# Kernel optimization log

Measured on AMD Instinct MI355X. Metric: run time of the kernel, lower is better.

The kernel has to match this reference:

```python
import jax, jax.numpy as jnp
import numpy as np

IN_CH = 256
NUM_ANCHORS = 9
NUM_CLASSES = 80
FEAT_SHAPES = [(4, IN_CH, 100, 100), (4, IN_CH, 50, 50), (4, IN_CH, 25, 25), (4, IN_CH, 13, 13), (4, IN_CH, 7, 7)]


def conv3x3(x, w, b):
    # x: [N,C,H,W], w: [O,I,3,3] (OIHW), stride 1, SAME padding
    y = jax.lax.conv_general_dilated(x, w, window_strides=(1, 1), padding='SAME',
                                     dimension_numbers=('NCHW', 'OIHW', 'NCHW'))
    return y + b[None, :, None, None]


def head_branch(x, conv_w, conv_b, out_w, out_b, K):
    for i in range(4):
        x = jax.nn.relu(conv3x3(x, conv_w[i], conv_b[i]))
    y = conv3x3(x, out_w, out_b)
    N, AK, H, W = y.shape
    A = AK // K
    return y.reshape(N, A, K, H, W).transpose(0, 3, 4, 1, 2).reshape(N, H * W * A, K)


def setup_inputs() -> dict:
    key = jax.random.key(0)
    ks = jax.random.split(key, 16)
    inp = {}
    for i, shp in enumerate(FEAT_SHAPES):
        inp[f'feat{i}'] = jax.random.normal(ks[i], shp, dtype=jnp.float32)
    std = 0.01  # torch init: normal(std=0.01), zero bias
    inp['cls_conv_w'] = jax.random.normal(ks[5], (4, IN_CH, IN_CH, 3, 3), dtype=jnp.float32) * std
    inp['cls_conv_b'] = jnp.zeros((4, IN_CH), dtype=jnp.float32)
    inp['cls_out_w'] = jax.random.normal(ks[6], (NUM_ANCHORS * NUM_CLASSES, IN_CH, 3, 3), dtype=jnp.float32) * std
    prior = 0.01
    inp['cls_out_b'] = jnp.full((NUM_ANCHORS * NUM_CLASSES,), -np.log((1.0 - prior) / prior), dtype=jnp.float32)
    inp['reg_conv_w'] = jax.random.normal(ks[7], (4, IN_CH, IN_CH, 3, 3), dtype=jnp.float32) * std
    inp['reg_conv_b'] = jnp.zeros((4, IN_CH), dtype=jnp.float32)
    inp['reg_out_w'] = jax.random.normal(ks[8], (NUM_ANCHORS * 4, IN_CH, 3, 3), dtype=jnp.float32) * std
    inp['reg_out_b'] = jnp.zeros((NUM_ANCHORS * 4,), dtype=jnp.float32)
    return inp


def reference(feat0, feat1, feat2, feat3, feat4,
              cls_conv_w, cls_conv_b, cls_out_w, cls_out_b,
              reg_conv_w, reg_conv_b, reg_out_w, reg_out_b):
    feats = [feat0, feat1, feat2, feat3, feat4]
    cls_logits = jnp.concatenate(
        [head_branch(f, cls_conv_w, cls_conv_b, cls_out_w, cls_out_b, NUM_CLASSES) for f in feats], axis=1)
    bbox_regression = jnp.concatenate(
        [head_branch(f, reg_conv_w, reg_conv_b, reg_out_w, reg_out_b, 4) for f in feats], axis=1)
    return cls_logits, bbox_regression
```

## Files before the change

kernel.cpp:

```cpp
#include <hip/hip_runtime.h>


typedef __bf16 v8bf __attribute__((ext_vector_type(8)));
typedef float f32x4 __attribute__((ext_vector_type(4)));

__device__ __forceinline__ v8bf zero8() {
  v8bf v;
#pragma unroll
  for (int j = 0; j < 8; ++j) v[j] = (__bf16)0.0f;
  return v;
}

__device__ __forceinline__ void glds16(const void* g, void* l) {
  __builtin_amdgcn_global_load_lds((const __attribute__((address_space(1))) unsigned int*)g,
                                   (__attribute__((address_space(3))) unsigned int*)l, 16, 0, 0);
}

struct Geo { int W, H, HW, pbase, obC, obR, t; };
__device__ __forceinline__ Geo decode(int r) {
  Geo g;
  if (r < 105)      { g.W=100;g.H=100;g.HW=10000;g.pbase=0;     g.obC=0;       g.obR=0;      g.t=r; }
  else if (r < 132) { g.W=50; g.H=50; g.HW=2500; g.pbase=40000; g.obC=7200000; g.obR=360000; g.t=r-105; }
  else if (r < 139) { g.W=25; g.H=25; g.HW=625;  g.pbase=50000; g.obC=9000000; g.obR=450000; g.t=r-132; }
  else if (r < 141) { g.W=13; g.H=13; g.HW=169;  g.pbase=52500; g.obC=9450000; g.obR=472500; g.t=r-139; }
  else              { g.W=7;  g.H=7;  g.HW=49;   g.pbase=53176; g.obC=9571680; g.obR=478584; g.t=r-141; }
  return g;
}

__global__ __launch_bounds__(256)
void prep_in(const float* __restrict__ f0, const float* __restrict__ f1,
             const float* __restrict__ f2, const float* __restrict__ f3,
             const float* __restrict__ f4, __bf16* __restrict__ dst)
{
  int oct = blockIdx.x * 256 + threadIdx.x;
  if (oct >= 1707904) return;
  int el = oct << 3;
  int c0 = el & 255;
  int pix = el >> 8;
  const float* s; int HW, hw, n;
  if (pix < 40000)      { s = f0; HW = 10000; int p = pix;         n = p / 10000; hw = p - n * 10000; }
  else if (pix < 50000) { s = f1; HW = 2500;  int p = pix - 40000; n = p / 2500;  hw = p - n * 2500;  }
  else if (pix < 52500) { s = f2; HW = 625;   int p = pix - 50000; n = p / 625;   hw = p - n * 625;   }
  else if (pix < 53176) { s = f3; HW = 169;   int p = pix - 52500; n = p / 169;   hw = p - n * 169;   }
  else                  { s = f4; HW = 49;    int p = pix - 53176; n = p / 49;    hw = p - n * 49;    }
  const float* sp = s + (n * 256 + c0) * HW + hw;
  v8bf v;
#pragma unroll
  for (int j = 0; j < 8; ++j) v[j] = (__bf16)sp[j * HW];
  *(v8bf*)(dst + el) = v;
}

__global__ __launch_bounds__(256)
void prep_w_all(const float* __restrict__ cls_w, const float* __restrict__ reg_w,
                const float* __restrict__ cls_ow, const float* __restrict__ reg_ow,
                __bf16* __restrict__ wb)
{
  int t = blockIdx.x * 256 + threadIdx.x;
  const float* src; __bf16* dst; int CO, within;
  if (t < 589824) {
    int tensor = t / 73728; within = t % 73728;
    src = tensor < 4 ? cls_w + tensor * 589824 : reg_w + (tensor - 4) * 589824;
    dst = wb + (size_t)tensor * 589824; CO = 256;
  } else if (t < 811008) {
    within = t - 589824; src = cls_ow; dst = wb + 8 * 589824; CO = 720;
  } else {
    within = t - 811008; src = reg_ow; dst = wb + 8 * 589824 + 1769472; CO = 36;
  }
  int p = within & 3; int xx = within >> 2;
  int co = xx & 127; xx >>= 7;
  int tap = xx % 9; xx /= 9;
  int cc = xx & 7; int nt = xx >> 3;
  int l = p ^ ((co >> 1) & 3);
  int cog = nt * 128 + co;
  v8bf v = zero8();
  if (cog < CO) {
    const float* sp = src + ((size_t)cog * 256 + cc * 32 + l * 8) * 9 + tap;
#pragma unroll
    for (int j = 0; j < 8; ++j) v[j] = (__bf16)sp[j * 9];
  }
  *(v8bf*)(dst + ((size_t)(((nt * 8 + cc) * 9 + tap) * 128 + co) * 32 + p * 8)) = v;
}

__device__ __forceinline__ void conv_core(const char* __restrict__ wsbase,
    unsigned so, unsigned zpoff, const char* __restrict__ wnt,
    int W, int H, int p0, int npx, f32x4 (&acc)[3][4])
{
  __shared__ __align__(16) char ldsA[28672];
  __shared__ __align__(16) char ldsB[24576];
  const int Wp = W + 2;
  const int pend = p0 + npx - 1;
  const int rowlo = p0 / W - 1;
  const int tid = threadIdx.x, lane = tid & 63, wv = tid >> 6;
  const int wn = wv & 1, wm = wv >> 1, la = lane & 15, kg = lane >> 4;

  unsigned offA[7];
#pragma unroll
  for (int j = 0; j < 7; ++j) {
    int pos = (wv * 7 + j) * 16 + (lane >> 2);
    int h = pos / Wp;
    int wc = pos - h * Wp - 1;
    int ar = rowlo + h;
    int pl = (lane & 3) ^ ((pos >> 1) & 3);
    bool ok = (ar >= 0) & (ar < H) & (wc >= 0) & (wc < W);
    offA[j] = ok ? (so + (unsigned)(ar * W + wc) * 512u + (unsigned)pl * 16u)
                 : (zpoff + (unsigned)(lane & 3) * 16u);
  }

  int pos0[3], fvalid[3];
#pragma unroll
  for (int f = 0; f < 3; ++f) {
    int fg = wm * 3 + f;
    fvalid[f] = (fg * 16 < npx);
    int p = p0 + fg * 16 + la; if (p > pend) p = pend;
    int h = p / W;
    pos0[f] = (h - rowlo) * Wp + (p - h * W + 1);
  }

  int boff[4];
#pragma unroll
  for (int nj = 0; nj < 4; ++nj) {
    int co = wn * 64 + nj * 16 + la;
    boff[nj] = (co << 6) + ((kg << 4) ^ (((co >> 1) & 3) << 4));
  }

  const char* bq = wnt + wv * 2048 + lane * 16;
  char* bd = (char*)ldsB + wv * 2048;

#pragma unroll
  for (int j = 0; j < 7; ++j) { glds16(wsbase + offA[j], (char*)ldsA + (wv * 7 + j) * 1024); offA[j] += 64u; }
  glds16(bq, bd); glds16(bq + 1024, bd + 1024);
  glds16(bq + 8192, bd + 8192); glds16(bq + 9216, bd + 9216);

  for (int cc = 0; cc < 8; ++cc) {
#pragma unroll
    for (int tap = 0; tap < 9; ++tap) {
      if (tap == 8) {
        if (cc == 7) { asm volatile("s_waitcnt vmcnt(0)" ::: "memory"); }
        else         { asm volatile("s_waitcnt vmcnt(2)" ::: "memory"); }
      } else         { asm volatile("s_waitcnt vmcnt(2)" ::: "memory"); }
      __builtin_amdgcn_s_barrier();
      if (tap == 0 && cc > 0) {
#pragma unroll
        for (int j = 0; j < 7; ++j) { glds16(wsbase + offA[j], (char*)ldsA + (wv * 7 + j) * 1024); offA[j] += 64u; }
        const char* bs = bq + (cc * 9 + 2) * 8192;
        glds16(bs, bd + 16384); glds16(bs + 1024, bd + 17408);
        asm volatile("s_waitcnt vmcnt(2)" ::: "memory");
        __builtin_amdgcn_s_barrier();
      } else {
        int q = cc * 9 + tap;
        if (q < 70) {
          const char* bs = bq + (q + 2) * 8192;
          char* d = bd + ((tap + 2) % 3) * 8192;
          glds16(bs, d); glds16(bs + 1024, d + 1024);
        }
      }
      const char* bbuf = (const char*)ldsB + (tap % 3) * 8192;
      v8bf bfr[4];
#pragma unroll
      for (int nj = 0; nj < 4; ++nj) bfr[nj] = *(const v8bf*)(bbuf + boff[nj]);
      const int dh = tap / 3 - 1, dw = tap % 3 - 1;
      const int dt = dh * Wp + dw;
      v8bf afr[3];
#pragma unroll
      for (int f = 0; f < 3; ++f)
        if (fvalid[f]) {
          int pos = pos0[f] + dt;
          afr[f] = *(const v8bf*)((const char*)ldsA + ((pos << 6) + ((kg << 4) ^ (((pos >> 1) & 3) << 4))));
        }
      __builtin_amdgcn_s_setprio(1);
#pragma unroll
      for (int f = 0; f < 3; ++f)
        if (fvalid[f])
#pragma unroll
          for (int nj = 0; nj < 4; ++nj)
            acc[f][nj] = __builtin_amdgcn_mfma_f32_16x16x32_bf16(afr[f], bfr[nj], acc[f][nj], 0, 0, 0);
      __builtin_amdgcn_s_setprio(0);
    }
  }
}

__global__ __launch_bounds__(256, 3)
void conv_tower(const char* __restrict__ wsbase,
                unsigned so0, __bf16* __restrict__ dst0, const __bf16* __restrict__ w0, const float* __restrict__ b0,
                unsigned so1, __bf16* __restrict__ dst1, const __bf16* __restrict__ w1, const float* __restrict__ b1,
                unsigned zpoff, int nb)
{
  int bid = blockIdx.x;
  int br = (nb == 2 && bid >= 1136) ? 1 : 0;
  bid -= br * 1136;
  unsigned soff = br ? so1 : so0;
  __bf16* dst = br ? dst1 : dst0;
  const __bf16* wt = br ? w1 : w0;
  const float* bias = br ? b1 : b0;

  int x = bid & 7, slot = bid >> 3;
  int nt = slot & 1, mtl = slot >> 1;
  int mt = x + (mtl << 3);
  int n = mt / 142, r = mt - n * 142;
  Geo g = decode(r);
  int p0 = g.t * 96;
  int npx = g.HW - p0; if (npx > 96) npx = 96;
  unsigned so = soff + (unsigned)(g.pbase + n * g.HW) * 512u;

  f32x4 acc[3][4];
#pragma unroll
  for (int f = 0; f < 3; ++f)
#pragma unroll
    for (int j = 0; j < 4; ++j)
#pragma unroll
      for (int k = 0; k < 4; ++k) acc[f][j][k] = 0.0f;

  conv_core(wsbase, so, zpoff, (const char*)(wt + nt * 294912), g.W, g.H, p0, npx, acc);

  int lane = threadIdx.x & 63, wv = threadIdx.x >> 6;
  int wm = wv >> 1, wn = wv & 1, la = lane & 15, kg = lane >> 4;
  size_t pixbase = (size_t)(g.pbase + n * g.HW + p0);
#pragma unroll
  for (int f = 0; f < 3; ++f) {
    int fg = wm * 3 + f;
    if (fg * 16 < npx) {
#pragma unroll
      for (int nj = 0; nj < 4; ++nj) {
        int cob = nt * 128 + wn * 64 + nj * 16 + la;
        float bs = bias[cob];
#pragma unroll
        for (int rr = 0; rr < 4; ++rr) {
          int pl = fg * 16 + kg * 4 + rr;
          if (pl < npx)
            dst[((pixbase + pl) << 8) + cob] = (__bf16)fmaxf(acc[f][nj][rr] + bs, 0.0f);
        }
      }
    }
  }
}

__global__ __launch_bounds__(256, 3)
void conv_out(const char* __restrict__ wsbase, unsigned soC, unsigned soR,
              float* __restrict__ out, const __bf16* __restrict__ wco, const float* __restrict__ bco,
              const __bf16* __restrict__ wro, const float* __restrict__ bro,
              unsigned zpoff, int mode)
{
  int bid = blockIdx.x;
  int isreg;
  if (mode == 2) { isreg = bid >= 3408; bid -= isreg ? 3408 : 0; }
  else isreg = (mode == 0);

  int x = bid & 7, slot = bid >> 3;
  int nt, mtl;
  if (!isreg) { nt = slot % 6; mtl = slot / 6; } else { nt = 0; mtl = slot; }
  int mt = x + mtl * 8;
  int n = mt / 142, r = mt - n * 142;
  Geo g = decode(r);
  int p0 = g.t * 96;
  int npx = g.HW - p0; if (npx > 96) npx = 96;
  unsigned so = (isreg ? soR : soC) + (unsigned)(g.pbase + n * g.HW) * 512u;
  const __bf16* wnt = isreg ? wro : (wco + nt * 294912);

  f32x4 acc[3][4];
#pragma unroll
  for (int f = 0; f < 3; ++f)
#pragma unroll
    for (int j = 0; j < 4; ++j)
#pragma unroll
      for (int k = 0; k < 4; ++k) acc[f][j][k] = 0.0f;

  conv_core(wsbase, so, zpoff, (const char*)wnt, g.W, g.H, p0, npx, acc);

  int lane = threadIdx.x & 63, wv = threadIdx.x >> 6;
  int wm = wv >> 1, wn = wv & 1, la = lane & 15, kg = lane >> 4;
#pragma unroll
  for (int f = 0; f < 3; ++f) {
    int fg = wm * 3 + f;
    if (fg * 16 < npx) {
#pragma unroll
      for (int nj = 0; nj < 4; ++nj) {
        int cob = nt * 128 + wn * 64 + nj * 16 + la;
#pragma unroll
        for (int rr = 0; rr < 4; ++rr) {
          int pl = fg * 16 + kg * 4 + rr;
          if (pl < npx) {
            int pix = p0 + pl;
            if (!isreg) {
              if (cob < 720)
                out[(size_t)n * 9606960 + g.obC + (size_t)pix * 720 + cob] = acc[f][nj][rr] + bco[cob];
            } else {
              if (cob < 36)
                out[38427840 + (size_t)n * 480348 + g.obR + (size_t)pix * 36 + cob] = acc[f][nj][rr] + bro[cob];
            }
          }
        }
      }
    }
  }
}

extern "C" void kernel_launch(void* const* d_in, const int* in_sizes, int n_in,
                              void* d_out, int out_size, void* d_ws, size_t ws_size,
                              hipStream_t stream) {
  (void)in_sizes; (void)n_in; (void)out_size;
  const float* feat0 = (const float*)d_in[0];
  const float* feat1 = (const float*)d_in[1];
  const float* feat2 = (const float*)d_in[2];
  const float* feat3 = (const float*)d_in[3];
  const float* feat4 = (const float*)d_in[4];
  const float* cls_w  = (const float*)d_in[5];
  const float* cls_b  = (const float*)d_in[6];
  const float* cls_ow = (const float*)d_in[7];
  const float* cls_ob = (const float*)d_in[8];
  const float* reg_w  = (const float*)d_in[9];
  const float* reg_b  = (const float*)d_in[10];
  const float* reg_ow = (const float*)d_in[11];
  const float* reg_ob = (const float*)d_in[12];
  float* out = (float*)d_out;

  const size_t ACT = 13663232;
  const size_t WSEG = 6782976;
  const char* wsbase = (const char*)d_ws;
  __bf16* base = (__bf16*)d_ws;

  bool fused = ws_size >= (5 * ACT + WSEG + 4096) * 2;
  int nact = fused ? 5 : 3;
  __bf16* A = base + ACT;
  __bf16* B = base + 2 * ACT;
  __bf16* C = fused ? base + 3 * ACT : A;
  __bf16* D = fused ? base + 4 * ACT : B;
  __bf16* wb = base + nact * ACT;

  __bf16* w_cls[4], *w_reg[4];
  for (int li = 0; li < 4; ++li) { w_cls[li] = wb + (size_t)li * 589824; w_reg[li] = wb + (size_t)(4 + li) * 589824; }
  __bf16* wco = wb + 8 * 589824;
  __bf16* wro = wco + 1769472;
  __bf16* zp = wro + 294912;

  unsigned off_in = 0;
  unsigned off_A = (unsigned)(ACT * 2);
  unsigned off_B = (unsigned)(ACT * 4);
  unsigned off_C = fused ? (unsigned)(ACT * 6) : off_A;
  unsigned off_D = fused ? (unsigned)(ACT * 8) : off_B;
  unsigned off_zp = (unsigned)((nact * ACT + WSEG) * 2);

  hipMemsetAsync(zp, 0, 8192, stream);
  prep_in<<<6672, 256, 0, stream>>>(feat0, feat1, feat2, feat3, feat4, base);
  prep_w_all<<<3312, 256, 0, stream>>>(cls_w, reg_w, cls_ow, reg_ow, wb);

  if (fused) {
    conv_tower<<<2272, 256, 0, stream>>>(wsbase, off_in, A, w_cls[0], cls_b + 0,   off_in, C, w_reg[0], reg_b + 0,   off_zp, 2);
    conv_tower<<<2272, 256, 0, stream>>>(wsbase, off_A,  B, w_cls[1], cls_b + 256, off_C,  D, w_reg[1], reg_b + 256, off_zp, 2);
    conv_tower<<<2272, 256, 0, stream>>>(wsbase, off_B,  A, w_cls[2], cls_b + 512, off_D,  C, w_reg[2], reg_b + 512, off_zp, 2);
    conv_tower<<<2272, 256, 0, stream>>>(wsbase, off_A,  B, w_cls[3], cls_b + 768, off_C,  D, w_reg[3], reg_b + 768, off_zp, 2);
    conv_out<<<3976, 256, 0, stream>>>(wsbase, off_B, off_D, out, wco, cls_ob, wro, reg_ob, off_zp, 2);
  } else {
    conv_tower<<<1136, 256, 0, stream>>>(wsbase, off_in, A, w_cls[0], cls_b + 0,   0, A, w_cls[0], cls_b, off_zp, 1);
    conv_tower<<<1136, 256, 0, stream>>>(wsbase, off_A,  B, w_cls[1], cls_b + 256, 0, A, w_cls[0], cls_b, off_zp, 1);
    conv_tower<<<1136, 256, 0, stream>>>(wsbase, off_B,  A, w_cls[2], cls_b + 512, 0, A, w_cls[0], cls_b, off_zp, 1);
    conv_tower<<<1136, 256, 0, stream>>>(wsbase, off_A,  B, w_cls[3], cls_b + 768, 0, A, w_cls[0], cls_b, off_zp, 1);
    conv_out<<<3408, 256, 0, stream>>>(wsbase, off_B, off_B, out, wco, cls_ob, wro, reg_ob, off_zp, 1);
    conv_tower<<<1136, 256, 0, stream>>>(wsbase, off_in, A, w_reg[0], reg_b + 0,   0, A, w_reg[0], reg_b, off_zp, 1);
    conv_tower<<<1136, 256, 0, stream>>>(wsbase, off_A,  B, w_reg[1], reg_b + 256, 0, A, w_reg[0], reg_b, off_zp, 1);
    conv_tower<<<1136, 256, 0, stream>>>(wsbase, off_B,  A, w_reg[2], reg_b + 512, 0, A, w_reg[0], reg_b, off_zp, 1);
    conv_tower<<<1136, 256, 0, stream>>>(wsbase, off_A,  B, w_reg[3], reg_b + 768, 0, A, w_reg[0], reg_b, off_zp, 1);
    conv_out<<<568, 256, 0, stream>>>(wsbase, off_B, off_B, out, wco, cls_ob, wro, reg_ob, off_zp, 0);
  }
}
```

Baseline: 1.029 ms.

## Use 128-pixel tiles for output conv and simplify LDS pipeline to double buffer

The output conv kernel now takes 128-pixel M tiles (4 fragments per wave) instead of 96, which cuts the number of blocks and reloads of the 720-channel weights. The shared conv core is templated on the fragment count. Its weight pipeline changes from a triple buffer with hand-placed vmcnt waits to a plain double buffer with __syncthreads. The XCD-aware block swizzle is dropped. The simpler sync adds full barriers and wait-for-all on every tap, which may cost latency hiding in the tower kernels, and the larger tile raises register and LDS use.

```diff
diff --git a/kernel.cpp b/kernel.cpp
--- a/kernel.cpp
+++ b/kernel.cpp
@@ -17,7 +17,17 @@
 }
 
 struct Geo { int W, H, HW, pbase, obC, obR, t; };
-__device__ __forceinline__ Geo decode(int r) {
+
+__device__ __forceinline__ Geo decode128(int r) {
+  Geo g;
+  if (r < 79)       { g.W=100;g.H=100;g.HW=10000;g.pbase=0;     g.obC=0;       g.obR=0;      g.t=r; }
+  else if (r < 99)  { g.W=50; g.H=50; g.HW=2500; g.pbase=40000; g.obC=7200000; g.obR=360000; g.t=r-79; }
+  else if (r < 104) { g.W=25; g.H=25; g.HW=625;  g.pbase=50000; g.obC=9000000; g.obR=450000; g.t=r-99; }
+  else if (r < 106) { g.W=13; g.H=13; g.HW=169;  g.pbase=52500; g.obC=9450000; g.obR=472500; g.t=r-104; }
+  else              { g.W=7;  g.H=7;  g.HW=49;   g.pbase=53176; g.obC=9571680; g.obR=478584; g.t=r-106; }
+  return g;
+}
+__device__ __forceinline__ Geo decode96(int r) {
   Geo g;
   if (r < 105)      { g.W=100;g.H=100;g.HW=10000;g.pbase=0;     g.obC=0;       g.obR=0;      g.t=r; }
   else if (r < 132) { g.W=50; g.H=50; g.HW=2500; g.pbase=40000; g.obC=7200000; g.obR=360000; g.t=r-105; }
@@ -81,22 +91,25 @@
   *(v8bf*)(dst + ((size_t)(((nt * 8 + cc) * 9 + tap) * 128 + co) * 32 + p * 8)) = v;
 }
 
+template<int NF>
 __device__ __forceinline__ void conv_core(const char* __restrict__ wsbase,
     unsigned so, unsigned zpoff, const char* __restrict__ wnt,
-    int W, int H, int p0, int npx, f32x4 (&acc)[3][4])
-{
-  __shared__ __align__(16) char ldsA[28672];
-  __shared__ __align__(16) char ldsB[24576];
+    int W, int H, int p0, int npx, f32x4 (&acc)[NF][4])
+{
+  constexpr int AG = (NF == 3) ? 7 : 8;
+  __shared__ __align__(16) char ldsA[AG * 4096];
+  __shared__ __align__(16) char ldsB[16384];
   const int Wp = W + 2;
   const int pend = p0 + npx - 1;
   const int rowlo = p0 / W - 1;
   const int tid = threadIdx.x, lane = tid & 63, wv = tid >> 6;
   const int wn = wv & 1, wm = wv >> 1, la = lane & 15, kg = lane >> 4;
-
-  unsigned offA[7];
-#pragma unroll
-  for (int j = 0; j < 7; ++j) {
-    int pos = (wv * 7 + j) * 16 + (lane >> 2);
+  const int i0 = wv * AG;
+
+  unsigned offA[AG];
+#pragma unroll
+  for (int j = 0; j < AG; ++j) {
+    int pos = (i0 + j) * 16 + (lane >> 2);
     int h = pos / Wp;
     int wc = pos - h * Wp - 1;
     int ar = rowlo + h;
@@ -106,10 +119,10 @@
                  : (zpoff + (unsigned)(lane & 3) * 16u);
   }
 
-  int pos0[3], fvalid[3];
-#pragma unroll
-  for (int f = 0; f < 3; ++f) {
-    int fg = wm * 3 + f;
+  int pos0[NF], fvalid[NF];
+#pragma unroll
+  for (int f = 0; f < NF; ++f) {
+    int fg = wm * NF + f;
     fvalid[f] = (fg * 16 < npx);
     int p = p0 + fg * 16 + la; if (p > pend) p = pend;
     int h = p / W;
@@ -126,57 +139,48 @@
   const char* bq = wnt + wv * 2048 + lane * 16;
   char* bd = (char*)ldsB + wv * 2048;
 
-#pragma unroll
-  for (int j = 0; j < 7; ++j) { glds16(wsbase + offA[j], (char*)ldsA + (wv * 7 + j) * 1024); offA[j] += 64u; }
-  glds16(bq, bd); glds16(bq + 1024, bd + 1024);
-  glds16(bq + 8192, bd + 8192); glds16(bq + 9216, bd + 9216);
+#define ISSUE_A() do { _Pragma("unroll") \
+    for (int j = 0; j < AG; ++j) { glds16(wsbase + offA[j], (char*)ldsA + (i0 + j) * 1024); offA[j] += 64u; } } while (0)
+#define ISSUE_B(q_, buf_) do { const char* s_ = bq + (q_) * 8192; \
+    char* d_ = bd + (buf_) * 8192; \
+    glds16(s_, d_); glds16(s_ + 1024, d_ + 1024); } while (0)
+
+  ISSUE_A();
+  ISSUE_B(0, 0);
+  int pb = 0;
 
   for (int cc = 0; cc < 8; ++cc) {
 #pragma unroll
     for (int tap = 0; tap < 9; ++tap) {
-      if (tap == 8) {
-        if (cc == 7) { asm volatile("s_waitcnt vmcnt(0)" ::: "memory"); }
-        else         { asm volatile("s_waitcnt vmcnt(2)" ::: "memory"); }
-      } else         { asm volatile("s_waitcnt vmcnt(2)" ::: "memory"); }
-      __builtin_amdgcn_s_barrier();
-      if (tap == 0 && cc > 0) {
-#pragma unroll
-        for (int j = 0; j < 7; ++j) { glds16(wsbase + offA[j], (char*)ldsA + (wv * 7 + j) * 1024); offA[j] += 64u; }
-        const char* bs = bq + (cc * 9 + 2) * 8192;
-        glds16(bs, bd + 16384); glds16(bs + 1024, bd + 17408);
-        asm volatile("s_waitcnt vmcnt(2)" ::: "memory");
-        __builtin_amdgcn_s_barrier();
-      } else {
-        int q = cc * 9 + tap;
-        if (q < 70) {
-          const char* bs = bq + (q + 2) * 8192;
-          char* d = bd + ((tap + 2) % 3) * 8192;
-          glds16(bs, d); glds16(bs + 1024, d + 1024);
-        }
-      }
-      const char* bbuf = (const char*)ldsB + (tap % 3) * 8192;
+      __syncthreads();
+      int q = cc * 9 + tap;
+      if (q < 71) ISSUE_B(q + 1, pb ^ 1);
       v8bf bfr[4];
 #pragma unroll
-      for (int nj = 0; nj < 4; ++nj) bfr[nj] = *(const v8bf*)(bbuf + boff[nj]);
+      for (int nj = 0; nj < 4; ++nj) bfr[nj] = *(const v8bf*)((const char*)ldsB + pb * 8192 + boff[nj]);
       const int dh = tap / 3 - 1, dw = tap % 3 - 1;
       const int dt = dh * Wp + dw;
-      v8bf afr[3];
-#pragma unroll
-      for (int f = 0; f < 3; ++f)
+      v8bf afr[NF];
+#pragma unroll
+      for (int f = 0; f < NF; ++f)
         if (fvalid[f]) {
           int pos = pos0[f] + dt;
           afr[f] = *(const v8bf*)((const char*)ldsA + ((pos << 6) + ((kg << 4) ^ (((pos >> 1) & 3) << 4))));
         }
       __builtin_amdgcn_s_setprio(1);
 #pragma unroll
-      for (int f = 0; f < 3; ++f)
+      for (int f = 0; f < NF; ++f)
         if (fvalid[f])
 #pragma unroll
           for (int nj = 0; nj < 4; ++nj)
             acc[f][nj] = __builtin_amdgcn_mfma_f32_16x16x32_bf16(afr[f], bfr[nj], acc[f][nj], 0, 0, 0);
       __builtin_amdgcn_s_setprio(0);
+      pb ^= 1;
+      if (tap == 8 && cc < 7) { __syncthreads(); ISSUE_A(); }
     }
   }
+#undef ISSUE_A
+#undef ISSUE_B
 }
 
 __global__ __launch_bounds__(256, 3)
@@ -193,11 +197,9 @@
   const __bf16* wt = br ? w1 : w0;
   const float* bias = br ? b1 : b0;
 
-  int x = bid & 7, slot = bid >> 3;
-  int nt = slot & 1, mtl = slot >> 1;
-  int mt = x + (mtl << 3);
+  int nt = bid & 1, mt = bid >> 1;
   int n = mt / 142, r = mt - n * 142;
-  Geo g = decode(r);
+  Geo g = decode96(r);
   int p0 = g.t * 96;
   int npx = g.HW - p0; if (npx > 96) npx = 96;
   unsigned so = soff + (unsigned)(g.pbase + n * g.HW) * 512u;
@@ -210,7 +212,7 @@
 #pragma unroll
       for (int k = 0; k < 4; ++k) acc[f][j][k] = 0.0f;
 
-  conv_core(wsbase, so, zpoff, (const char*)(wt + nt * 294912), g.W, g.H, p0, npx, acc);
+  conv_core<3>(wsbase, so, zpoff, (const char*)(wt + nt * 294912), g.W, g.H, p0, npx, acc);
 
   int lane = threadIdx.x & 63, wv = threadIdx.x >> 6;
   int wm = wv >> 1, wn = wv & 1, la = lane & 15, kg = lane >> 4;
@@ -242,35 +244,33 @@
 {
   int bid = blockIdx.x;
   int isreg;
-  if (mode == 2) { isreg = bid >= 3408; bid -= isreg ? 3408 : 0; }
+  if (mode == 2) { isreg = bid >= 2568; bid -= isreg ? 2568 : 0; }
   else isreg = (mode == 0);
 
-  int x = bid & 7, slot = bid >> 3;
-  int nt, mtl;
-  if (!isreg) { nt = slot % 6; mtl = slot / 6; } else { nt = 0; mtl = slot; }
-  int mt = x + mtl * 8;
-  int n = mt / 142, r = mt - n * 142;
-  Geo g = decode(r);
-  int p0 = g.t * 96;
-  int npx = g.HW - p0; if (npx > 96) npx = 96;
+  int nt, mt;
+  if (!isreg) { nt = bid % 6; mt = bid / 6; } else { nt = 0; mt = bid; }
+  int n = mt / 107, r = mt - n * 107;
+  Geo g = decode128(r);
+  int p0 = g.t << 7;
+  int npx = g.HW - p0; if (npx > 128) npx = 128;
   unsigned so = (isreg ? soR : soC) + (unsigned)(g.pbase + n * g.HW) * 512u;
   const __bf16* wnt = isreg ? wro : (wco + nt * 294912);
 
-  f32x4 acc[3][4];
-#pragma unroll
-  for (int f = 0; f < 3; ++f)
+  f32x4 acc[4][4];
+#pragma unroll
+  for (int f = 0; f < 4; ++f)
 #pragma unroll
     for (int j = 0; j < 4; ++j)
 #pragma unroll
       for (int k = 0; k < 4; ++k) acc[f][j][k] = 0.0f;
 
-  conv_core(wsbase, so, zpoff, (const char*)wnt, g.W, g.H, p0, npx, acc);
+  conv_core<4>(wsbase, so, zpoff, (const char*)wnt, g.W, g.H, p0, npx, acc);
 
   int lane = threadIdx.x & 63, wv = threadIdx.x >> 6;
   int wm = wv >> 1, wn = wv & 1, la = lane & 15, kg = lane >> 4;
 #pragma unroll
-  for (int f = 0; f < 3; ++f) {
-    int fg = wm * 3 + f;
+  for (int f = 0; f < 4; ++f) {
+    int fg = wm * 4 + f;
     if (fg * 16 < npx) {
 #pragma unroll
       for (int nj = 0; nj < 4; ++nj) {
@@ -348,17 +348,17 @@
     conv_tower<<<2272, 256, 0, stream>>>(wsbase, off_A,  B, w_cls[1], cls_b + 256, off_C,  D, w_reg[1], reg_b + 256, off_zp, 2);
     conv_tower<<<2272, 256, 0, stream>>>(wsbase, off_B,  A, w_cls[2], cls_b + 512, off_D,  C, w_reg[2], reg_b + 512, off_zp, 2);
     conv_tower<<<2272, 256, 0, stream>>>(wsbase, off_A,  B, w_cls[3], cls_b + 768, off_C,  D, w_reg[3], reg_b + 768, off_zp, 2);
-    conv_out<<<3976, 256, 0, stream>>>(wsbase, off_B, off_D, out, wco, cls_ob, wro, reg_ob, off_zp, 2);
+    conv_out<<<2996, 256, 0, stream>>>(wsbase, off_B, off_D, out, wco, cls_ob, wro, reg_ob, off_zp, 2);
   } else {
     conv_tower<<<1136, 256, 0, stream>>>(wsbase, off_in, A, w_cls[0], cls_b + 0,   0, A, w_cls[0], cls_b, off_zp, 1);
     conv_tower<<<1136, 256, 0, stream>>>(wsbase, off_A,  B, w_cls[1], cls_b + 256, 0, A, w_cls[0], cls_b, off_zp, 1);
     conv_tower<<<1136, 256, 0, stream>>>(wsbase, off_B,  A, w_cls[2], cls_b + 512, 0, A, w_cls[0], cls_b, off_zp, 1);
     conv_tower<<<1136, 256, 0, stream>>>(wsbase, off_A,  B, w_cls[3], cls_b + 768, 0, A, w_cls[0], cls_b, off_zp, 1);
-    conv_out<<<3408, 256, 0, stream>>>(wsbase, off_B, off_B, out, wco, cls_ob, wro, reg_ob, off_zp, 1);
+    conv_out<<<2568, 256, 0, stream>>>(wsbase, off_B, off_B, out, wco, cls_ob, wro, reg_ob, off_zp, 1);
     conv_tower<<<1136, 256, 0, stream>>>(wsbase, off_in, A, w_reg[0], reg_b + 0,   0, A, w_reg[0], reg_b, off_zp, 1);
     conv_tower<<<1136, 256, 0, stream>>>(wsbase, off_A,  B, w_reg[1], reg_b + 256, 0, A, w_reg[0], reg_b, off_zp, 1);
     conv_tower<<<1136, 256, 0, stream>>>(wsbase, off_B,  A, w_reg[2], reg_b + 512, 0, A, w_reg[0], reg_b, off_zp, 1);
     conv_tower<<<1136, 256, 0, stream>>>(wsbase, off_A,  B, w_reg[3], reg_b + 768, 0, A, w_reg[0], reg_b, off_zp, 1);
-    conv_out<<<568, 256, 0, stream>>>(wsbase, off_B, off_B, out, wco, cls_ob, wro, reg_ob, off_zp, 0);
-  }
-}
+    conv_out<<<428, 256, 0, stream>>>(wsbase, off_B, off_B, out, wco, cls_ob, wro, reg_ob, off_zp, 0);
+  }
+}
```

Measured after the change: 1.069 ms. 3.9% more time.

## Use 128-pixel tiles for output convs and split cls/reg output kernels

Applied to the files above, without the earlier changes.

Adds a separate conv core for the output convolutions with 128-pixel M tiles (4 fragments per wave) and a new tile decode, and splits the combined output kernel into dedicated cls and reg kernels. The larger tile is meant to raise weight reuse and cut the number of output blocks. The tower kernel's launch bounds also drop from 3 to 2 blocks per SM, which may lower occupancy. The new output core drops the s_setprio hints and uses a different LDS split.

```diff
diff --git a/kernel.cpp b/kernel.cpp
--- a/kernel.cpp
+++ b/kernel.cpp
@@ -17,7 +17,17 @@
 }
 
 struct Geo { int W, H, HW, pbase, obC, obR, t; };
-__device__ __forceinline__ Geo decode(int r) {
+
+__device__ __forceinline__ Geo decode128(int r) {
+  Geo g;
+  if (r < 79)       { g.W=100;g.H=100;g.HW=10000;g.pbase=0;     g.obC=0;       g.obR=0;      g.t=r; }
+  else if (r < 99)  { g.W=50; g.H=50; g.HW=2500; g.pbase=40000; g.obC=7200000; g.obR=360000; g.t=r-79; }
+  else if (r < 104) { g.W=25; g.H=25; g.HW=625;  g.pbase=50000; g.obC=9000000; g.obR=450000; g.t=r-99; }
+  else if (r < 106) { g.W=13; g.H=13; g.HW=169;  g.pbase=52500; g.obC=9450000; g.obR=472500; g.t=r-104; }
+  else              { g.W=7;  g.H=7;  g.HW=49;   g.pbase=53176; g.obC=9571680; g.obR=478584; g.t=r-106; }
+  return g;
+}
+__device__ __forceinline__ Geo decode96(int r) {
   Geo g;
   if (r < 105)      { g.W=100;g.H=100;g.HW=10000;g.pbase=0;     g.obC=0;       g.obR=0;      g.t=r; }
   else if (r < 132) { g.W=50; g.H=50; g.HW=2500; g.pbase=40000; g.obC=7200000; g.obR=360000; g.t=r-105; }
@@ -81,7 +91,7 @@
   *(v8bf*)(dst + ((size_t)(((nt * 8 + cc) * 9 + tap) * 128 + co) * 32 + p * 8)) = v;
 }
 
-__device__ __forceinline__ void conv_core(const char* __restrict__ wsbase,
+__device__ __forceinline__ void conv_core_t(const char* __restrict__ wsbase,
     unsigned so, unsigned zpoff, const char* __restrict__ wnt,
     int W, int H, int p0, int npx, f32x4 (&acc)[3][4])
 {
@@ -179,15 +189,103 @@
   }
 }
 
-__global__ __launch_bounds__(256, 3)
+__device__ __forceinline__ void conv_core_o(const char* __restrict__ wsbase,
+    unsigned so, unsigned zpoff, const char* __restrict__ wnt,
+    int W, int H, int p0, int npx, f32x4 (&acc)[4][4])
+{
+  __shared__ __align__(16) char ldsA[32768];
+  __shared__ __align__(16) char ldsB[16384];
+  const int Wp = W + 2;
+  const int pend = p0 + npx - 1;
+  const int rowlo = p0 / W - 1;
+  const int tid = threadIdx.x, lane = tid & 63, wv = tid >> 6;
+  const int wn = wv & 1, wm = wv >> 1, la = lane & 15, kg = lane >> 4;
+  const int i0 = wv * 8;
+
+  unsigned offA[8];
+#pragma unroll
+  for (int j = 0; j < 8; ++j) {
+    int pos = (i0 + j) * 16 + (lane >> 2);
+    int h = pos / Wp;
+    int wc = pos - h * Wp - 1;
+    int ar = rowlo + h;
+    int pl = (lane & 3) ^ ((pos >> 1) & 3);
+    bool ok = (ar >= 0) & (ar < H) & (wc >= 0) & (wc < W);
+    offA[j] = ok ? (so + (unsigned)(ar * W + wc) * 512u + (unsigned)pl * 16u)
+                 : (zpoff + (unsigned)(lane & 3) * 16u);
+  }
+
+  int pos0[4], fvalid[4];
+#pragma unroll
+  for (int f = 0; f < 4; ++f) {
+    int fg = wm * 4 + f;
+    fvalid[f] = (fg * 16 < npx);
+    int p = p0 + fg * 16 + la; if (p > pend) p = pend;
+    int h = p / W;
+    pos0[f] = (h - rowlo) * Wp + (p - h * W + 1);
+  }
+
+  int boff[4];
+#pragma unroll
+  for (int nj = 0; nj < 4; ++nj) {
+    int co = wn * 64 + nj * 16 + la;
+    boff[nj] = (co << 6) + ((kg << 4) ^ (((co >> 1) & 3) << 4));
+  }
+
+  const char* bq = wnt + wv * 2048 + lane * 16;
+  char* bd = (char*)ldsB + wv * 2048;
+
+#define ISSUE_AO() do { _Pragma("unroll") \
+    for (int j = 0; j < 8; ++j) { glds16(wsbase + offA[j], (char*)ldsA + (i0 + j) * 1024); offA[j] += 64u; } } while (0)
+#define ISSUE_BO(q_, buf_) do { const char* s_ = bq + (q_) * 8192; \
+    char* d_ = bd + (buf_) * 8192; \
+    glds16(s_, d_); glds16(s_ + 1024, d_ + 1024); } while (0)
+
+  ISSUE_AO();
+  ISSUE_BO(0, 0);
+  int pb = 0;
+
+  for (int cc = 0; cc < 8; ++cc) {
+#pragma unroll
+    for (int tap = 0; tap < 9; ++tap) {
+      __syncthreads();
+      int q = cc * 9 + tap;
+      if (q < 71) ISSUE_BO(q + 1, pb ^ 1);
+      v8bf bfr[4];
+#pragma unroll
+      for (int nj = 0; nj < 4; ++nj) bfr[nj] = *(const v8bf*)((const char*)ldsB + pb * 8192 + boff[nj]);
+      const int dh = tap / 3 - 1, dw = tap % 3 - 1;
+      const int dt = dh * Wp + dw;
+      v8bf afr[4];
+#pragma unroll
+      for (int f = 0; f < 4; ++f)
+        if (fvalid[f]) {
+          int pos = pos0[f] + dt;
+          afr[f] = *(const v8bf*)((const char*)ldsA + ((pos << 6) + ((kg << 4) ^ (((pos >> 1) & 3) << 4))));
+        }
+#pragma unroll
+      for (int f = 0; f < 4; ++f)
+        if (fvalid[f])
+#pragma unroll
+          for (int nj = 0; nj < 4; ++nj)
+            acc[f][nj] = __builtin_amdgcn_mfma_f32_16x16x32_bf16(afr[f], bfr[nj], acc[f][nj], 0, 0, 0);
+      pb ^= 1;
+      if (tap == 8 && cc < 7) { __syncthreads(); ISSUE_AO(); }
+    }
+  }
+#undef ISSUE_AO
+#undef ISSUE_BO
+}
+
+__global__ __launch_bounds__(256, 2)
 void conv_tower(const char* __restrict__ wsbase,
                 unsigned so0, __bf16* __restrict__ dst0, const __bf16* __restrict__ w0, const float* __restrict__ b0,
                 unsigned so1, __bf16* __restrict__ dst1, const __bf16* __restrict__ w1, const float* __restrict__ b1,
-                unsigned zpoff, int nb)
+                unsigned zpoff, int half)
 {
   int bid = blockIdx.x;
-  int br = (nb == 2 && bid >= 1136) ? 1 : 0;
-  bid -= br * 1136;
+  int br = bid >= half;
+  bid -= br ? half : 0;
   unsigned soff = br ? so1 : so0;
   __bf16* dst = br ? dst1 : dst0;
   const __bf16* wt = br ? w1 : w0;
@@ -197,7 +295,7 @@
   int nt = slot & 1, mtl = slot >> 1;
   int mt = x + (mtl << 3);
   int n = mt / 142, r = mt - n * 142;
-  Geo g = decode(r);
+  Geo g = decode96(r);
   int p0 = g.t * 96;
   int npx = g.HW - p0; if (npx > 96) npx = 96;
   unsigned so = soff + (unsigned)(g.pbase + n * g.HW) * 512u;
@@ -210,7 +308,7 @@
 #pragma unroll
       for (int k = 0; k < 4; ++k) acc[f][j][k] = 0.0f;
 
-  conv_core(wsbase, so, zpoff, (const char*)(wt + nt * 294912), g.W, g.H, p0, npx, acc);
+  conv_core_t(wsbase, so, zpoff, (const char*)(wt + nt * 294912), g.W, g.H, p0, npx, acc);
 
   int lane = threadIdx.x & 63, wv = threadIdx.x >> 6;
   int wm = wv >> 1, wn = wv & 1, la = lane & 15, kg = lane >> 4;
@@ -235,57 +333,91 @@
 }
 
 __global__ __launch_bounds__(256, 3)
-void conv_out(const char* __restrict__ wsbase, unsigned soC, unsigned soR,
-              float* __restrict__ out, const __bf16* __restrict__ wco, const float* __restrict__ bco,
-              const __bf16* __restrict__ wro, const float* __restrict__ bro,
-              unsigned zpoff, int mode)
+void conv_cls_out(const char* __restrict__ wsbase, unsigned soA,
+                  float* __restrict__ out, const __bf16* __restrict__ wco,
+                  const float* __restrict__ bco, unsigned zpoff)
 {
   int bid = blockIdx.x;
-  int isreg;
-  if (mode == 2) { isreg = bid >= 3408; bid -= isreg ? 3408 : 0; }
-  else isreg = (mode == 0);
-
-  int x = bid & 7, slot = bid >> 3;
-  int nt, mtl;
-  if (!isreg) { nt = slot % 6; mtl = slot / 6; } else { nt = 0; mtl = slot; }
-  int mt = x + mtl * 8;
-  int n = mt / 142, r = mt - n * 142;
-  Geo g = decode(r);
-  int p0 = g.t * 96;
-  int npx = g.HW - p0; if (npx > 96) npx = 96;
-  unsigned so = (isreg ? soR : soC) + (unsigned)(g.pbase + n * g.HW) * 512u;
-  const __bf16* wnt = isreg ? wro : (wco + nt * 294912);
-
-  f32x4 acc[3][4];
-#pragma unroll
-  for (int f = 0; f < 3; ++f)
+  int nt = bid % 6, mt = bid / 6;
+  int n = mt / 107, r = mt - n * 107;
+  Geo g = decode128(r);
+  int p0 = g.t << 7;
+  int npx = g.HW - p0; if (npx > 128) npx = 128;
+  unsigned so = soA + (unsigned)(g.pbase + n * g.HW) * 512u;
+
+  f32x4 acc[4][4];
+#pragma unroll
+  for (int f = 0; f < 4; ++f)
 #pragma unroll
     for (int j = 0; j < 4; ++j)
 #pragma unroll
       for (int k = 0; k < 4; ++k) acc[f][j][k] = 0.0f;
 
-  conv_core(wsbase, so, zpoff, (const char*)wnt, g.W, g.H, p0, npx, acc);
+  conv_core_o(wsbase, so, zpoff, (const char*)(wco + nt * 294912), g.W, g.H, p0, npx, acc);
 
   int lane = threadIdx.x & 63, wv = threadIdx.x >> 6;
   int wm = wv >> 1, wn = wv & 1, la = lane & 15, kg = lane >> 4;
 #pragma unroll
-  for (int f = 0; f < 3; ++f) {
-    int fg = wm * 3 + f;
+  for (int f = 0; f < 4; ++f) {
+    int fg = wm * 4 + f;
     if (fg * 16 < npx) {
 #pragma unroll
       for (int nj = 0; nj < 4; ++nj) {
         int cob = nt * 128 + wn * 64 + nj * 16 + la;
-#pragma unroll
-        for (int rr = 0; rr < 4; ++rr) {
-          int pl = fg * 16 + kg * 4 + rr;
-          if (pl < npx) {
-            int pix = p0 + pl;
-            if (!isreg) {
-              if (cob < 720)
-                out[(size_t)n * 9606960 + g.obC + (size_t)pix * 720 + cob] = acc[f][nj][rr] + bco[cob];
-            } else {
-              if (cob < 36)
-                out[38427840 + (size_t)n * 480348 + g.obR + (size_t)pix * 36 + cob] = acc[f][nj][rr] + bro[cob];
+        if (cob < 720) {
+          float bs = bco[cob];
+#pragma unroll
+          for (int rr = 0; rr < 4; ++rr) {
+            int pl = fg * 16 + kg * 4 + rr;
+            if (pl < npx) {
+              int pix = p0 + pl;
+              out[(size_t)n * 9606960 + g.obC + (size_t)pix * 720 + cob] = acc[f][nj][rr] + bs;
+            }
+          }
+        }
+      }
+    }
+  }
+}
+
+__global__ __launch_bounds__(256, 3)
+void conv_reg_out(const char* __restrict__ wsbase, unsigned soA,
+                  float* __restrict__ out, const __bf16* __restrict__ wro,
+                  const float* __restrict__ bro, unsigned zpoff)
+{
+  int mt = blockIdx.x;
+  int n = mt / 107, r = mt - n * 107;
+  Geo g = decode128(r);
+  int p0 = g.t << 7;
+  int npx = g.HW - p0; if (npx > 128) npx = 128;
+  unsigned so = soA + (unsigned)(g.pbase + n * g.HW) * 512u;
+
+  f32x4 acc[4][4];
+#pragma unroll
+  for (int f = 0; f < 4; ++f)
+#pragma unroll
+    for (int j = 0; j < 4; ++j)
+#pragma unroll
+      for (int k = 0; k < 4; ++k) acc[f][j][k] = 0.0f;
+
+  conv_core_o(wsbase, so, zpoff, (const char*)wro, g.W, g.H, p0, npx, acc);
+
+  int lane = threadIdx.x & 63, wv = threadIdx.x >> 6;
+  int wm = wv >> 1, wn = wv & 1, la = lane & 15, kg = lane >> 4;
+#pragma unroll
+  for (int f = 0; f < 4; ++f) {
+    int fg = wm * 4 + f;
+    if (fg * 16 < npx) {
+#pragma unroll
+      for (int nj = 0; nj < 4; ++nj) {
+        int cob = wn * 64 + nj * 16 + la;
+        if (cob < 36) {
+#pragma unroll
+          for (int rr = 0; rr < 4; ++rr) {
+            int pl = fg * 16 + kg * 4 + rr;
+            if (pl < npx) {
+              int pix = p0 + pl;
+              out[38427840 + (size_t)n * 480348 + g.obR + (size_t)pix * 36 + cob] = acc[f][nj][rr] + bro[cob];
             }
           }
         }
@@ -344,21 +476,22 @@
   prep_w_all<<<3312, 256, 0, stream>>>(cls_w, reg_w, cls_ow, reg_ow, wb);
 
   if (fused) {
-    conv_tower<<<2272, 256, 0, stream>>>(wsbase, off_in, A, w_cls[0], cls_b + 0,   off_in, C, w_reg[0], reg_b + 0,   off_zp, 2);
-    conv_tower<<<2272, 256, 0, stream>>>(wsbase, off_A,  B, w_cls[1], cls_b + 256, off_C,  D, w_reg[1], reg_b + 256, off_zp, 2);
-    conv_tower<<<2272, 256, 0, stream>>>(wsbase, off_B,  A, w_cls[2], cls_b + 512, off_D,  C, w_reg[2], reg_b + 512, off_zp, 2);
-    conv_tower<<<2272, 256, 0, stream>>>(wsbase, off_A,  B, w_cls[3], cls_b + 768, off_C,  D, w_reg[3], reg_b + 768, off_zp, 2);
-    conv_out<<<3976, 256, 0, stream>>>(wsbase, off_B, off_D, out, wco, cls_ob, wro, reg_ob, off_zp, 2);
+    conv_tower<<<2272, 256, 0, stream>>>(wsbase, off_in, A, w_cls[0], cls_b + 0,   off_in, C, w_reg[0], reg_b + 0,   off_zp, 1136);
+    conv_tower<<<2272, 256, 0, stream>>>(wsbase, off_A,  B, w_cls[1], cls_b + 256, off_C,  D, w_reg[1], reg_b + 256, off_zp, 1136);
+    conv_tower<<<2272, 256, 0, stream>>>(wsbase, off_B,  A, w_cls[2], cls_b + 512, off_D,  C, w_reg[2], reg_b + 512, off_zp, 1136);
+    conv_tower<<<2272, 256, 0, stream>>>(wsbase, off_A,  B, w_cls[3], cls_b + 768, off_C,  D, w_reg[3], reg_b + 768, off_zp, 1136);
+    conv_cls_out<<<2568, 256, 0, stream>>>(wsbase, off_B, out, wco, cls_ob, off_zp);
+    conv_reg_out<<<428, 256, 0, stream>>>(wsbase, off_D, out, wro, reg_ob, off_zp);
   } else {
-    conv_tower<<<1136, 256, 0, stream>>>(wsbase, off_in, A, w_cls[0], cls_b + 0,   0, A, w_cls[0], cls_b, off_zp, 1);
-    conv_tower<<<1136, 256, 0, stream>>>(wsbase, off_A,  B, w_cls[1], cls_b + 256, 0, A, w_cls[0], cls_b, off_zp, 1);
-    conv_tower<<<1136, 256, 0, stream>>>(wsbase, off_B,  A, w_cls[2], cls_b + 512, 0, A, w_cls[0], cls_b, off_zp, 1);
-    conv_tower<<<1136, 256, 0, stream>>>(wsbase, off_A,  B, w_cls[3], cls_b + 768, 0, A, w_cls[0], cls_b, off_zp, 1);
-    conv_out<<<3408, 256, 0, stream>>>(wsbase, off_B, off_B, out, wco, cls_ob, wro, reg_ob, off_zp, 1);
-    conv_tower<<<1136, 256, 0, stream>>>(wsbase, off_in, A, w_reg[0], reg_b + 0,   0, A, w_reg[0], reg_b, off_zp, 1);
-    conv_tower<<<1136, 256, 0, stream>>>(wsbase, off_A,  B, w_reg[1], reg_b + 256, 0, A, w_reg[0], reg_b, off_zp, 1);
-    conv_tower<<<1136, 256, 0, stream>>>(wsbase, off_B,  A, w_reg[2], reg_b + 512, 0, A, w_reg[0], reg_b, off_zp, 1);
-    conv_tower<<<1136, 256, 0, stream>>>(wsbase, off_A,  B, w_reg[3], reg_b + 768, 0, A, w_reg[0], reg_b, off_zp, 1);
-    conv_out<<<568, 256, 0, stream>>>(wsbase, off_B, off_B, out, wco, cls_ob, wro, reg_ob, off_zp, 0);
-  }
-}
+    conv_tower<<<1136, 256, 0, stream>>>(wsbase, off_in, A, w_cls[0], cls_b + 0,   off_in, A, w_cls[0], cls_b, off_zp, 1136);
+    conv_tower<<<1136, 256, 0, stream>>>(wsbase, off_A,  B, w_cls[1], cls_b + 256, off_A,  B, w_cls[1], cls_b, off_zp, 1136);
+    conv_tower<<<1136, 256, 0, stream>>>(wsbase, off_B,  A, w_cls[2], cls_b + 512, off_B,  A, w_cls[2], cls_b, off_zp, 1136);
+    conv_tower<<<1136, 256, 0, stream>>>(wsbase, off_A,  B, w_cls[3], cls_b + 768, off_A,  B, w_cls[3], cls_b, off_zp, 1136);
+    conv_cls_out<<<2568, 256, 0, stream>>>(wsbase, off_B, out, wco, cls_ob, off_zp);
+    conv_tower<<<1136, 256, 0, stream>>>(wsbase, off_in, A, w_reg[0], reg_b + 0,   off_in, A, w_reg[0], reg_b, off_zp, 1136);
+    conv_tower<<<1136, 256, 0, stream>>>(wsbase, off_A,  B, w_reg[1], reg_b + 256, off_A,  B, w_reg[1], reg_b, off_zp, 1136);
+    conv_tower<<<1136, 256, 0, stream>>>(wsbase, off_B,  A, w_reg[2], reg_b + 512, off_B,  A, w_reg[2], reg_b, off_zp, 1136);
+    conv_tower<<<1136, 256, 0, stream>>>(wsbase, off_A,  B, w_reg[3], reg_b + 768, off_A,  B, w_reg[3], reg_b, off_zp, 1136);
+    conv_reg_out<<<428, 256, 0, stream>>>(wsbase, off_B, out, wro, reg_ob, off_zp);
+  }
+}
```

New measurement: 1.016 ms. About the same (-1.2%).
